# Optimization experiments

Hardware: AMD Instinct MI355X
Metric: run time of the kernel (lower is better)

Reference implementation:

```python
import jax, jax.numpy as jnp
import numpy as np

EPS = 1e-6
ALPHA = 0.1
BETA = 0.25


def setup_inputs() -> dict:
    key = jax.random.key(0)
    k1, k2, k3 = jax.random.split(key, 3)
    B, C, D = 4096, 256, 128
    x = jax.random.normal(k1, (B, D), dtype=jnp.float32)
    prev_q = jax.random.normal(k2, (B, D), dtype=jnp.float32)
    codes = jax.random.normal(k3, (1, C, D), dtype=jnp.float32)
    return {"x": x, "prev_q": prev_q, "codes": codes}


def compute_distance(x, codes):
    # x: (B, D); codes: (1, C, D) or (B, 1, D) -> (B, C) / (B, 1); metric='l2'
    return jnp.sum((x[:, None, :] - codes) ** 2, axis=-1)


def get_rotation_matrix(u, v, eps=EPS):
    # u: (B, D) normalized; v: (D,) normalized -> R: (B, D, D)
    B, D = u.shape
    uvT = u[:, :, None] * v[None, None, :]          # (B, D, D) = u v^T
    vuT = v[None, :, None] * u[:, None, :]          # (B, D, D) = v u^T
    A = uvT - vuT
    A2 = jnp.einsum('bik,bkj->bij', A, A)
    dot = jnp.einsum('bd,d->b', u, v)[:, None, None]
    I = jnp.eye(D, dtype=u.dtype)
    return I + A + A2 / (1.0 + dot + eps)


def reference(x, prev_q, codes):
    B, D = x.shape
    v = jnp.ones((D,), dtype=x.dtype) / jnp.sqrt(jnp.asarray(D, x.dtype))
    # F.normalize(prev_q, dim=-1, eps=1e-6)
    n = jnp.linalg.norm(prev_q, axis=-1, keepdims=True)
    u = prev_q / jnp.maximum(n, EPS)
    R = get_rotation_matrix(u, v)
    # x_canonical = R^T x
    x_canonical = jnp.einsum('bji,bj->bi', R, x)
    raw_distances = compute_distance(x_canonical, codes)        # (B, C)
    distances = raw_distances / D / ALPHA
    # eval path: argmin + gather
    indices = jnp.argmin(distances, axis=-1)                    # (B,)
    quantized_canonical = codes[0][indices]                     # (B, D)
    quantized = jnp.einsum('bij,bj->bi', R, quantized_canonical)
    loss_commit = compute_distance(x, jax.lax.stop_gradient(quantized)[:, None, :]).mean()
    loss_codebook = compute_distance(jax.lax.stop_gradient(x), quantized[:, None, :]).mean()
    loss = loss_commit + BETA * loss_codebook
    return quantized, indices, loss
```

## Files before the change

kernel.cpp:

```cpp
#include <hip/hip_runtime.h>

#define BD 4096
#define CD 256
#define DD 128
#define RB 16
#define TB 1024
#define SF 132

__global__ __launch_bounds__(TB) void rq_fused(
    const float* __restrict__ x,
    const float* __restrict__ pq,
    const float* __restrict__ codes,
    float* __restrict__ out)
{
    __shared__ float code_s[CD * SF];
    __shared__ float xc_s[RB * SF];
    __shared__ float row_c[RB], row_s[RB], row_invn[RB];
    __shared__ int   row_idx[RB];
    __shared__ float red_v[RB * 4];
    __shared__ int   red_i[RB * 4];
    __shared__ float loss_s[RB];

    const int tid  = threadIdx.x;
    const int wv   = tid >> 6;
    const int lane = tid & 63;
    const int row0 = blockIdx.x * RB;
    const float INV_SQRT_D = 0.088388347648318447f;

    {
        const float4* src = (const float4*)codes;
        #pragma unroll
        for (int k = 0; k < 8; k += 4) {
            const float4 t0 = src[(k + 0) * TB + tid];
            const float4 t1 = src[(k + 1) * TB + tid];
            const float4 t2 = src[(k + 2) * TB + tid];
            const float4 t3 = src[(k + 3) * TB + tid];
            int f;
            f = (k + 0) * TB + tid; *(float4*)(code_s + (f >> 5) * SF + (f & 31) * 4) = t0;
            f = (k + 1) * TB + tid; *(float4*)(code_s + (f >> 5) * SF + (f & 31) * 4) = t1;
            f = (k + 2) * TB + tid; *(float4*)(code_s + (f >> 5) * SF + (f & 31) * 4) = t2;
            f = (k + 3) * TB + tid; *(float4*)(code_s + (f >> 5) * SF + (f & 31) * 4) = t3;
        }
    }

    {
        const int r = wv;
        const size_t grow = (size_t)(row0 + r);
        const float2 xv = ((const float2*)(x  + grow * DD))[lane];
        const float2 pv = ((const float2*)(pq + grow * DD))[lane];
        float s0 = pv.x * pv.x + pv.y * pv.y;
        float s1 = pv.x + pv.y;
        float s2 = xv.x + xv.y;
        float s3 = pv.x * xv.x + pv.y * xv.y;
        #pragma unroll
        for (int m = 32; m > 0; m >>= 1) {
            s0 += __shfl_xor(s0, m);
            s1 += __shfl_xor(s1, m);
            s2 += __shfl_xor(s2, m);
            s3 += __shfl_xor(s3, m);
        }
        const float invn = 1.0f / fmaxf(sqrtf(s0), 1e-6f);
        const float b = s2 * INV_SQRT_D;
        const float a = s3 * invn;
        const float c = s1 * invn * INV_SQRT_D;
        const float s = 1.0f / (1.0f + c + 1e-6f);
        const float au = -b + s * (c * b - a);
        const float av =  a + s * (c * a - b);
        xc_s[r * SF + 2 * lane]     = xv.x + au * (pv.x * invn) + av * INV_SQRT_D;
        xc_s[r * SF + 2 * lane + 1] = xv.y + au * (pv.y * invn) + av * INV_SQRT_D;
        if (lane == 0) { row_c[r] = c; row_s[r] = s; row_invn[r] = invn; }
    }
    __syncthreads();

    const int rg = wv & 3;
    const int cq = wv >> 2;
    const int ci = cq * 64 + lane;
    const float* cp = code_s + ci * SF;
    const float* xb = xc_s + (rg * 4) * SF;
    float a0 = 0.f, a1 = 0.f, a2 = 0.f, a3 = 0.f;

    #pragma unroll 4
    for (int i = 0; i < 32; ++i) {
        const float4 q  = *(const float4*)(cp + i * 4);
        const float4 v0 = *(const float4*)(xb + 0 * SF + i * 4);
        const float4 v1 = *(const float4*)(xb + 1 * SF + i * 4);
        const float4 v2 = *(const float4*)(xb + 2 * SF + i * 4);
        const float4 v3 = *(const float4*)(xb + 3 * SF + i * 4);
        float dx;
        dx = v0.x - q.x; a0 = fmaf(dx, dx, a0);
        dx = v0.y - q.y; a0 = fmaf(dx, dx, a0);
        dx = v0.z - q.z; a0 = fmaf(dx, dx, a0);
        dx = v0.w - q.w; a0 = fmaf(dx, dx, a0);
        dx = v1.x - q.x; a1 = fmaf(dx, dx, a1);
        dx = v1.y - q.y; a1 = fmaf(dx, dx, a1);
        dx = v1.z - q.z; a1 = fmaf(dx, dx, a1);
        dx = v1.w - q.w; a1 = fmaf(dx, dx, a1);
        dx = v2.x - q.x; a2 = fmaf(dx, dx, a2);
        dx = v2.y - q.y; a2 = fmaf(dx, dx, a2);
        dx = v2.z - q.z; a2 = fmaf(dx, dx, a2);
        dx = v2.w - q.w; a2 = fmaf(dx, dx, a2);
        dx = v3.x - q.x; a3 = fmaf(dx, dx, a3);
        dx = v3.y - q.y; a3 = fmaf(dx, dx, a3);
        dx = v3.z - q.z; a3 = fmaf(dx, dx, a3);
        dx = v3.w - q.w; a3 = fmaf(dx, dx, a3);
    }

    float bv[4] = {a0, a1, a2, a3};
    int   bi[4] = {ci, ci, ci, ci};
    #pragma unroll
    for (int m = 1; m < 64; m <<= 1) {
        #pragma unroll
        for (int rr = 0; rr < 4; ++rr) {
            const float ov = __shfl_xor(bv[rr], m);
            const int   oi = __shfl_xor(bi[rr], m);
            if (ov < bv[rr] || (ov == bv[rr] && oi < bi[rr])) { bv[rr] = ov; bi[rr] = oi; }
        }
    }
    if (lane == 0) {
        #pragma unroll
        for (int rr = 0; rr < 4; ++rr) {
            red_v[(rg * 4 + rr) * 4 + cq] = bv[rr];
            red_i[(rg * 4 + rr) * 4 + cq] = bi[rr];
        }
    }
    __syncthreads();
    if (tid < RB) {
        float v0 = red_v[tid * 4]; int i0 = red_i[tid * 4];
        #pragma unroll
        for (int k = 1; k < 4; ++k) {
            const float ov = red_v[tid * 4 + k];
            const int   oi = red_i[tid * 4 + k];
            if (ov < v0 || (ov == v0 && oi < i0)) { v0 = ov; i0 = oi; }
        }
        row_idx[tid] = i0;
        out[(size_t)BD * DD + row0 + tid] = (float)i0;
    }
    __syncthreads();

    {
        const int r = wv;
        const int qi = row_idx[r];
        const float invn = row_invn[r];
        const float c = row_c[r];
        const float s = row_s[r];
        const size_t grow = (size_t)(row0 + r);
        const float2 q = ((const float2*)(code_s + qi * SF))[lane];
        const float2 p = ((const float2*)(pq + grow * DD))[lane];
        float pd = p.x * q.x + p.y * q.y;
        float ws = q.x + q.y;
        #pragma unroll
        for (int m = 32; m > 0; m >>= 1) {
            pd += __shfl_xor(pd, m);
            ws += __shfl_xor(ws, m);
        }
        const float pp = pd * invn;
        const float w  = ws * INV_SQRT_D;
        const float bu  =  w + s * (c * w - pp);
        const float bvv = -pp + s * (c * pp - w);
        float2 o;
        o.x = q.x + bu * (p.x * invn) + bvv * INV_SQRT_D;
        o.y = q.y + bu * (p.y * invn) + bvv * INV_SQRT_D;
        ((float2*)(out + grow * DD))[lane] = o;

        const float2 xv = ((const float2*)(x + grow * DD))[lane];
        float dx = xv.x - o.x;
        float ls = dx * dx;
        dx = xv.y - o.y;
        ls = fmaf(dx, dx, ls);
        #pragma unroll
        for (int m = 32; m > 0; m >>= 1) ls += __shfl_xor(ls, m);
        if (lane == 0) loss_s[r] = ls;
    }
    __syncthreads();
    if (tid == 0) {
        float tot = 0.f;
        #pragma unroll
        for (int r = 0; r < RB; ++r) tot += loss_s[r];
        atomicAdd(out + (size_t)BD * DD + BD, tot * (1.25f / (float)BD));
    }
}

extern "C" void kernel_launch(void* const* d_in, const int* in_sizes, int n_in,
                              void* d_out, int out_size, void* d_ws, size_t ws_size,
                              hipStream_t stream) {
    const float* xin   = (const float*)d_in[0];
    const float* prevq = (const float*)d_in[1];
    const float* codes = (const float*)d_in[2];
    float* out = (float*)d_out;
    hipMemsetAsync((void*)(out + (size_t)BD * DD + BD), 0, sizeof(float), stream);
    rq_fused<<<BD / RB, TB, 0, stream>>>(xin, prevq, codes, out);
}
```

Before: 77.47 us.

## Expand L2 distance algebraically using code norms and dot products with x and prev_q

Replaces the explicit canonical-vector distance with an expansion: ||c||^2 - 2 c·x - k1 c·p - k2 sum(c). The per-code norms and sums are precomputed in shared memory, and x and prev_q rows are read directly from global memory with wave-uniform addresses instead of from a shared xc buffer. This doubles the dot products per inner step and adds an extra sync and precompute pass. It also changes floating-point rounding, which could flip argmin decisions on near-ties.

```diff
diff --git a/kernel.cpp b/kernel.cpp
--- a/kernel.cpp
+++ b/kernel.cpp
@@ -14,8 +14,9 @@
     float* __restrict__ out)
 {
     __shared__ float code_s[CD * SF];
-    __shared__ float xc_s[RB * SF];
-    __shared__ float row_c[RB], row_s[RB], row_invn[RB];
+    __shared__ float cn2_s[CD];
+    __shared__ float csum_s[CD];
+    __shared__ float row_c[RB], row_s[RB], row_invn[RB], row_k1[RB], row_k2[RB];
     __shared__ int   row_idx[RB];
     __shared__ float red_v[RB * 4];
     __shared__ int   red_i[RB * 4];
@@ -66,47 +67,80 @@
         const float s = 1.0f / (1.0f + c + 1e-6f);
         const float au = -b + s * (c * b - a);
         const float av =  a + s * (c * a - b);
-        xc_s[r * SF + 2 * lane]     = xv.x + au * (pv.x * invn) + av * INV_SQRT_D;
-        xc_s[r * SF + 2 * lane + 1] = xv.y + au * (pv.y * invn) + av * INV_SQRT_D;
-        if (lane == 0) { row_c[r] = c; row_s[r] = s; row_invn[r] = invn; }
+        if (lane == 0) {
+            row_c[r] = c; row_s[r] = s; row_invn[r] = invn;
+            row_k1[r] = 2.0f * au * invn;
+            row_k2[r] = 2.0f * av * INV_SQRT_D;
+        }
+    }
+    __syncthreads();
+
+    if (tid < CD) {
+        const float* cp = code_s + tid * SF;
+        float n2 = 0.f, sm = 0.f;
+        #pragma unroll 8
+        for (int i = 0; i < 32; ++i) {
+            const float4 q = *(const float4*)(cp + i * 4);
+            n2 = fmaf(q.x, q.x, n2); n2 = fmaf(q.y, q.y, n2);
+            n2 = fmaf(q.z, q.z, n2); n2 = fmaf(q.w, q.w, n2);
+            sm += q.x + q.y + q.z + q.w;
+        }
+        cn2_s[tid] = n2; csum_s[tid] = sm;
     }
     __syncthreads();
 
     const int rg = wv & 3;
     const int cq = wv >> 2;
     const int ci = cq * 64 + lane;
+    const float cn2 = cn2_s[ci];
+    const float csm = csum_s[ci];
+    const int r0 = rg * 4;
+    const float k10 = row_k1[r0 + 0], k20 = row_k2[r0 + 0];
+    const float k11 = row_k1[r0 + 1], k21 = row_k2[r0 + 1];
+    const float k12 = row_k1[r0 + 2], k22 = row_k2[r0 + 2];
+    const float k13 = row_k1[r0 + 3], k23 = row_k2[r0 + 3];
+    const int grbase = __builtin_amdgcn_readfirstlane(row0 + r0);
+    const float* xb = x  + (size_t)grbase * DD;
+    const float* pb = pq + (size_t)grbase * DD;
     const float* cp = code_s + ci * SF;
-    const float* xb = xc_s + (rg * 4) * SF;
-    float a0 = 0.f, a1 = 0.f, a2 = 0.f, a3 = 0.f;
-
-    #pragma unroll 4
+    float ax0 = 0.f, ax1 = 0.f, ax2 = 0.f, ax3 = 0.f;
+    float ap0 = 0.f, ap1 = 0.f, ap2 = 0.f, ap3 = 0.f;
+
+    #pragma unroll 2
     for (int i = 0; i < 32; ++i) {
-        const float4 q  = *(const float4*)(cp + i * 4);
-        const float4 v0 = *(const float4*)(xb + 0 * SF + i * 4);
-        const float4 v1 = *(const float4*)(xb + 1 * SF + i * 4);
-        const float4 v2 = *(const float4*)(xb + 2 * SF + i * 4);
-        const float4 v3 = *(const float4*)(xb + 3 * SF + i * 4);
-        float dx;
-        dx = v0.x - q.x; a0 = fmaf(dx, dx, a0);
-        dx = v0.y - q.y; a0 = fmaf(dx, dx, a0);
-        dx = v0.z - q.z; a0 = fmaf(dx, dx, a0);
-        dx = v0.w - q.w; a0 = fmaf(dx, dx, a0);
-        dx = v1.x - q.x; a1 = fmaf(dx, dx, a1);
-        dx = v1.y - q.y; a1 = fmaf(dx, dx, a1);
-        dx = v1.z - q.z; a1 = fmaf(dx, dx, a1);
-        dx = v1.w - q.w; a1 = fmaf(dx, dx, a1);
-        dx = v2.x - q.x; a2 = fmaf(dx, dx, a2);
-        dx = v2.y - q.y; a2 = fmaf(dx, dx, a2);
-        dx = v2.z - q.z; a2 = fmaf(dx, dx, a2);
-        dx = v2.w - q.w; a2 = fmaf(dx, dx, a2);
-        dx = v3.x - q.x; a3 = fmaf(dx, dx, a3);
-        dx = v3.y - q.y; a3 = fmaf(dx, dx, a3);
-        dx = v3.z - q.z; a3 = fmaf(dx, dx, a3);
-        dx = v3.w - q.w; a3 = fmaf(dx, dx, a3);
-    }
-
-    float bv[4] = {a0, a1, a2, a3};
-    int   bi[4] = {ci, ci, ci, ci};
+        const float4 cv = *(const float4*)(cp + i * 4);
+        const float4 x0 = *(const float4*)(xb + 0 * DD + i * 4);
+        const float4 x1 = *(const float4*)(xb + 1 * DD + i * 4);
+        const float4 x2 = *(const float4*)(xb + 2 * DD + i * 4);
+        const float4 x3 = *(const float4*)(xb + 3 * DD + i * 4);
+        const float4 p0 = *(const float4*)(pb + 0 * DD + i * 4);
+        const float4 p1 = *(const float4*)(pb + 1 * DD + i * 4);
+        const float4 p2 = *(const float4*)(pb + 2 * DD + i * 4);
+        const float4 p3 = *(const float4*)(pb + 3 * DD + i * 4);
+        ax0 = fmaf(cv.x, x0.x, ax0); ax0 = fmaf(cv.y, x0.y, ax0);
+        ax0 = fmaf(cv.z, x0.z, ax0); ax0 = fmaf(cv.w, x0.w, ax0);
+        ap0 = fmaf(cv.x, p0.x, ap0); ap0 = fmaf(cv.y, p0.y, ap0);
+        ap0 = fmaf(cv.z, p0.z, ap0); ap0 = fmaf(cv.w, p0.w, ap0);
+        ax1 = fmaf(cv.x, x1.x, ax1); ax1 = fmaf(cv.y, x1.y, ax1);
+        ax1 = fmaf(cv.z, x1.z, ax1); ax1 = fmaf(cv.w, x1.w, ax1);
+        ap1 = fmaf(cv.x, p1.x, ap1); ap1 = fmaf(cv.y, p1.y, ap1);
+        ap1 = fmaf(cv.z, p1.z, ap1); ap1 = fmaf(cv.w, p1.w, ap1);
+        ax2 = fmaf(cv.x, x2.x, ax2); ax2 = fmaf(cv.y, x2.y, ax2);
+        ax2 = fmaf(cv.z, x2.z, ax2); ax2 = fmaf(cv.w, x2.w, ax2);
+        ap2 = fmaf(cv.x, p2.x, ap2); ap2 = fmaf(cv.y, p2.y, ap2);
+        ap2 = fmaf(cv.z, p2.z, ap2); ap2 = fmaf(cv.w, p2.w, ap2);
+        ax3 = fmaf(cv.x, x3.x, ax3); ax3 = fmaf(cv.y, x3.y, ax3);
+        ax3 = fmaf(cv.z, x3.z, ax3); ax3 = fmaf(cv.w, x3.w, ax3);
+        ap3 = fmaf(cv.x, p3.x, ap3); ap3 = fmaf(cv.y, p3.y, ap3);
+        ap3 = fmaf(cv.z, p3.z, ap3); ap3 = fmaf(cv.w, p3.w, ap3);
+    }
+
+    float bv[4]; int bi[4];
+    bv[0] = cn2 - 2.0f * ax0 - k10 * ap0 - k20 * csm;
+    bv[1] = cn2 - 2.0f * ax1 - k11 * ap1 - k21 * csm;
+    bv[2] = cn2 - 2.0f * ax2 - k12 * ap2 - k22 * csm;
+    bv[3] = cn2 - 2.0f * ax3 - k13 * ap3 - k23 * csm;
+    bi[0] = ci; bi[1] = ci; bi[2] = ci; bi[3] = ci;
     #pragma unroll
     for (int m = 1; m < 64; m <<= 1) {
         #pragma unroll
@@ -119,8 +153,8 @@
     if (lane == 0) {
         #pragma unroll
         for (int rr = 0; rr < 4; ++rr) {
-            red_v[(rg * 4 + rr) * 4 + cq] = bv[rr];
-            red_i[(rg * 4 + rr) * 4 + cq] = bi[rr];
+            red_v[(r0 + rr) * 4 + cq] = bv[rr];
+            red_i[(r0 + rr) * 4 + cq] = bi[rr];
         }
     }
     __syncthreads();
```

Result: slower. 81.04 us (+4.6%).

## Use dot-product expansion for L2 distances with split-K across wave halves

Applied to the files above, without the earlier changes.

Replaces the direct (x-c)^2 accumulation with ||c||^2 - 2·x·c, precomputing code norms in shared memory. Each wave now computes a 4-row × 2-code register tile over half of D, and the two halves are merged through shared memory that reuses the codebook buffer. Because that buffer is overwritten, the final gather reads the chosen code from global memory. This trades fewer subtracts and better register reuse for extra barriers, the partial-sum exchange and a small risk of argmin ties changing under the different rounding.

```diff
diff --git a/kernel.cpp b/kernel.cpp
--- a/kernel.cpp
+++ b/kernel.cpp
@@ -13,13 +13,25 @@
     const float* __restrict__ codes,
     float* __restrict__ out)
 {
-    __shared__ float code_s[CD * SF];
-    __shared__ float xc_s[RB * SF];
-    __shared__ float row_c[RB], row_s[RB], row_invn[RB];
-    __shared__ int   row_idx[RB];
-    __shared__ float red_v[RB * 4];
-    __shared__ int   red_i[RB * 4];
-    __shared__ float loss_s[RB];
+    __shared__ __align__(16) char pool[CD * SF * 4
+                                       + RB * DD * 4
+                                       + CD * 4
+                                       + RB * 4 * 4
+                                       + RB * 4
+                                       + RB * 2 * 8
+                                       + RB * 4];
+    float* code_s = (float*)pool;
+    float* mbuf   = (float*)pool;
+    float* xc_s   = (float*)(pool + CD * SF * 4);
+    float* cn2_s  = xc_s + RB * DD;
+    float* row_c  = cn2_s + CD;
+    float* row_s  = row_c + RB;
+    float* row_invn = row_s + RB;
+    float* row_pad  = row_invn + RB;  (void)row_pad;
+    int*   row_idx  = (int*)(row_invn + 2 * RB);
+    float* red_v    = (float*)(row_idx + RB);
+    int*   red_i    = (int*)(red_v + RB * 2);
+    float* loss_s   = (float*)(red_i + RB * 2);
 
     const int tid  = threadIdx.x;
     const int wv   = tid >> 6;
@@ -66,72 +78,114 @@
         const float s = 1.0f / (1.0f + c + 1e-6f);
         const float au = -b + s * (c * b - a);
         const float av =  a + s * (c * a - b);
-        xc_s[r * SF + 2 * lane]     = xv.x + au * (pv.x * invn) + av * INV_SQRT_D;
-        xc_s[r * SF + 2 * lane + 1] = xv.y + au * (pv.y * invn) + av * INV_SQRT_D;
+        float2 o;
+        o.x = xv.x + au * (pv.x * invn) + av * INV_SQRT_D;
+        o.y = xv.y + au * (pv.y * invn) + av * INV_SQRT_D;
+        ((float2*)(xc_s + r * DD))[lane] = o;
         if (lane == 0) { row_c[r] = c; row_s[r] = s; row_invn[r] = invn; }
     }
     __syncthreads();
 
-    const int rg = wv & 3;
-    const int cq = wv >> 2;
-    const int ci = cq * 64 + lane;
-    const float* cp = code_s + ci * SF;
-    const float* xb = xc_s + (rg * 4) * SF;
+    {
+        const int c = tid >> 2, q = tid & 3;
+        const float* cp = code_s + c * SF + q * 32;
+        float n2 = 0.f;
+        #pragma unroll
+        for (int i = 0; i < 8; ++i) {
+            const float4 v = *(const float4*)(cp + i * 4);
+            n2 = fmaf(v.x, v.x, n2); n2 = fmaf(v.y, v.y, n2);
+            n2 = fmaf(v.z, v.z, n2); n2 = fmaf(v.w, v.w, n2);
+        }
+        n2 += __shfl_xor(n2, 1);
+        n2 += __shfl_xor(n2, 2);
+        if (q == 0) cn2_s[c] = n2;
+    }
+    __syncthreads();
+
+    const int wgrp = wv & 7, half = wv >> 3;
+    const int rg = wgrp & 3, ch = wgrp >> 2;
+    const float* cb = code_s + (ch * 128 + lane) * SF + half * 64;
+    const float* xb = xc_s + (rg * 4) * DD + half * 64;
     float a0 = 0.f, a1 = 0.f, a2 = 0.f, a3 = 0.f;
+    float a4 = 0.f, a5 = 0.f, a6 = 0.f, a7 = 0.f;
 
     #pragma unroll 4
-    for (int i = 0; i < 32; ++i) {
-        const float4 q  = *(const float4*)(cp + i * 4);
-        const float4 v0 = *(const float4*)(xb + 0 * SF + i * 4);
-        const float4 v1 = *(const float4*)(xb + 1 * SF + i * 4);
-        const float4 v2 = *(const float4*)(xb + 2 * SF + i * 4);
-        const float4 v3 = *(const float4*)(xb + 3 * SF + i * 4);
-        float dx;
-        dx = v0.x - q.x; a0 = fmaf(dx, dx, a0);
-        dx = v0.y - q.y; a0 = fmaf(dx, dx, a0);
-        dx = v0.z - q.z; a0 = fmaf(dx, dx, a0);
-        dx = v0.w - q.w; a0 = fmaf(dx, dx, a0);
-        dx = v1.x - q.x; a1 = fmaf(dx, dx, a1);
-        dx = v1.y - q.y; a1 = fmaf(dx, dx, a1);
-        dx = v1.z - q.z; a1 = fmaf(dx, dx, a1);
-        dx = v1.w - q.w; a1 = fmaf(dx, dx, a1);
-        dx = v2.x - q.x; a2 = fmaf(dx, dx, a2);
-        dx = v2.y - q.y; a2 = fmaf(dx, dx, a2);
-        dx = v2.z - q.z; a2 = fmaf(dx, dx, a2);
-        dx = v2.w - q.w; a2 = fmaf(dx, dx, a2);
-        dx = v3.x - q.x; a3 = fmaf(dx, dx, a3);
-        dx = v3.y - q.y; a3 = fmaf(dx, dx, a3);
-        dx = v3.z - q.z; a3 = fmaf(dx, dx, a3);
-        dx = v3.w - q.w; a3 = fmaf(dx, dx, a3);
-    }
-
-    float bv[4] = {a0, a1, a2, a3};
-    int   bi[4] = {ci, ci, ci, ci};
-    #pragma unroll
-    for (int m = 1; m < 64; m <<= 1) {
-        #pragma unroll
-        for (int rr = 0; rr < 4; ++rr) {
-            const float ov = __shfl_xor(bv[rr], m);
-            const int   oi = __shfl_xor(bi[rr], m);
-            if (ov < bv[rr] || (ov == bv[rr] && oi < bi[rr])) { bv[rr] = ov; bi[rr] = oi; }
-        }
-    }
-    if (lane == 0) {
-        #pragma unroll
-        for (int rr = 0; rr < 4; ++rr) {
-            red_v[(rg * 4 + rr) * 4 + cq] = bv[rr];
-            red_i[(rg * 4 + rr) * 4 + cq] = bi[rr];
+    for (int i = 0; i < 16; ++i) {
+        const float4 c0 = *(const float4*)(cb + i * 4);
+        const float4 c1 = *(const float4*)(cb + 64 * SF + i * 4);
+        const float4 x0 = *(const float4*)(xb + 0 * DD + i * 4);
+        const float4 x1 = *(const float4*)(xb + 1 * DD + i * 4);
+        const float4 x2 = *(const float4*)(xb + 2 * DD + i * 4);
+        const float4 x3 = *(const float4*)(xb + 3 * DD + i * 4);
+        a0 = fmaf(c0.x, x0.x, a0); a0 = fmaf(c0.y, x0.y, a0);
+        a0 = fmaf(c0.z, x0.z, a0); a0 = fmaf(c0.w, x0.w, a0);
+        a1 = fmaf(c1.x, x0.x, a1); a1 = fmaf(c1.y, x0.y, a1);
+        a1 = fmaf(c1.z, x0.z, a1); a1 = fmaf(c1.w, x0.w, a1);
+        a2 = fmaf(c0.x, x1.x, a2); a2 = fmaf(c0.y, x1.y, a2);
+        a2 = fmaf(c0.z, x1.z, a2); a2 = fmaf(c0.w, x1.w, a2);
+        a3 = fmaf(c1.x, x1.x, a3); a3 = fmaf(c1.y, x1.y, a3);
+        a3 = fmaf(c1.z, x1.z, a3); a3 = fmaf(c1.w, x1.w, a3);
+        a4 = fmaf(c0.x, x2.x, a4); a4 = fmaf(c0.y, x2.y, a4);
+        a4 = fmaf(c0.z, x2.z, a4); a4 = fmaf(c0.w, x2.w, a4);
+        a5 = fmaf(c1.x, x2.x, a5); a5 = fmaf(c1.y, x2.y, a5);
+        a5 = fmaf(c1.z, x2.z, a5); a5 = fmaf(c1.w, x2.w, a5);
+        a6 = fmaf(c0.x, x3.x, a6); a6 = fmaf(c0.y, x3.y, a6);
+        a6 = fmaf(c0.z, x3.z, a6); a6 = fmaf(c0.w, x3.w, a6);
+        a7 = fmaf(c1.x, x3.x, a7); a7 = fmaf(c1.y, x3.y, a7);
+        a7 = fmaf(c1.z, x3.z, a7); a7 = fmaf(c1.w, x3.w, a7);
+    }
+
+    __syncthreads();
+    if (half == 1) {
+        float* mb = mbuf + ((size_t)wgrp * 64 + lane) * 8;
+        float4 v;
+        v.x = a0; v.y = a1; v.z = a2; v.w = a3; *(float4*)(mb)     = v;
+        v.x = a4; v.y = a5; v.z = a6; v.w = a7; *(float4*)(mb + 4) = v;
+    }
+    __syncthreads();
+    if (half == 0) {
+        const float* mb = mbuf + ((size_t)wgrp * 64 + lane) * 8;
+        const float4 m0 = *(const float4*)(mb);
+        const float4 m1 = *(const float4*)(mb + 4);
+        a0 += m0.x; a1 += m0.y; a2 += m0.z; a3 += m0.w;
+        a4 += m1.x; a5 += m1.y; a6 += m1.z; a7 += m1.w;
+        const int c0i = ch * 128 + lane;
+        const int c1i = c0i + 64;
+        const float cn20 = cn2_s[c0i];
+        const float cn21 = cn2_s[c1i];
+        float bv[4]; int bi[4];
+        {
+            const float s00 = fmaf(-2.f, a0, cn20), s01 = fmaf(-2.f, a1, cn21);
+            const float s10 = fmaf(-2.f, a2, cn20), s11 = fmaf(-2.f, a3, cn21);
+            const float s20 = fmaf(-2.f, a4, cn20), s21 = fmaf(-2.f, a5, cn21);
+            const float s30 = fmaf(-2.f, a6, cn20), s31 = fmaf(-2.f, a7, cn21);
+            if (s01 < s00) { bv[0] = s01; bi[0] = c1i; } else { bv[0] = s00; bi[0] = c0i; }
+            if (s11 < s10) { bv[1] = s11; bi[1] = c1i; } else { bv[1] = s10; bi[1] = c0i; }
+            if (s21 < s20) { bv[2] = s21; bi[2] = c1i; } else { bv[2] = s20; bi[2] = c0i; }
+            if (s31 < s30) { bv[3] = s31; bi[3] = c1i; } else { bv[3] = s30; bi[3] = c0i; }
+        }
+        #pragma unroll
+        for (int m = 1; m < 64; m <<= 1) {
+            #pragma unroll
+            for (int rr = 0; rr < 4; ++rr) {
+                const float ov = __shfl_xor(bv[rr], m);
+                const int   oi = __shfl_xor(bi[rr], m);
+                if (ov < bv[rr] || (ov == bv[rr] && oi < bi[rr])) { bv[rr] = ov; bi[rr] = oi; }
+            }
+        }
+        if (lane == 0) {
+            #pragma unroll
+            for (int rr = 0; rr < 4; ++rr) {
+                red_v[(rg * 4 + rr) * 2 + ch] = bv[rr];
+                red_i[(rg * 4 + rr) * 2 + ch] = bi[rr];
+            }
         }
     }
     __syncthreads();
     if (tid < RB) {
-        float v0 = red_v[tid * 4]; int i0 = red_i[tid * 4];
-        #pragma unroll
-        for (int k = 1; k < 4; ++k) {
-            const float ov = red_v[tid * 4 + k];
-            const int   oi = red_i[tid * 4 + k];
-            if (ov < v0 || (ov == v0 && oi < i0)) { v0 = ov; i0 = oi; }
-        }
+        float v0 = red_v[tid * 2]; int i0 = red_i[tid * 2];
+        const float v1 = red_v[tid * 2 + 1]; const int i1 = red_i[tid * 2 + 1];
+        if (v1 < v0 || (v1 == v0 && i1 < i0)) { v0 = v1; i0 = i1; }
         row_idx[tid] = i0;
         out[(size_t)BD * DD + row0 + tid] = (float)i0;
     }
@@ -144,7 +198,7 @@
         const float c = row_c[r];
         const float s = row_s[r];
         const size_t grow = (size_t)(row0 + r);
-        const float2 q = ((const float2*)(code_s + qi * SF))[lane];
+        const float2 q = ((const float2*)(codes + (size_t)qi * DD))[lane];
         const float2 p = ((const float2*)(pq + grow * DD))[lane];
         float pd = p.x * q.x + p.y * q.y;
         float ws = q.x + q.y;
```

Result: faster. 74.45 us (-3.9%).

## Register-tile distance as dot products with split-K across waves and shared-memory merge

Applied to the files above, without the earlier changes.

The distance loop becomes a 4x4 register tile of row-by-code dot products plus code norms, computed as ||c||^2 - 2 x·c. The D dimension is split across four wave groups, and partial sums are merged through shared memory that reuses the codebook buffer. Only one wave group then runs the argmin, which removes the separate cross-wave reduction stage. Because the codebook buffer is overwritten, the final gather now reads the chosen code from global memory. In exchange there is an extra synchronization and merge pass, and the dot-product form can change argmin tie-breaking in floating point.

```diff
diff --git a/kernel.cpp b/kernel.cpp
--- a/kernel.cpp
+++ b/kernel.cpp
@@ -13,13 +13,19 @@
     const float* __restrict__ codes,
     float* __restrict__ out)
 {
-    __shared__ float code_s[CD * SF];
-    __shared__ float xc_s[RB * SF];
-    __shared__ float row_c[RB], row_s[RB], row_invn[RB];
-    __shared__ int   row_idx[RB];
-    __shared__ float red_v[RB * 4];
-    __shared__ int   red_i[RB * 4];
-    __shared__ float loss_s[RB];
+    __shared__ __align__(16) char pool[CD * SF * 4
+                                       + RB * DD * 4
+                                       + RB * 3 * 4
+                                       + RB * 4
+                                       + RB * 4];
+    float* code_s   = (float*)pool;
+    float* mbuf     = (float*)pool;
+    float* xc_s     = (float*)(pool + CD * SF * 4);
+    float* row_c    = xc_s + RB * DD;
+    float* row_s    = row_c + RB;
+    float* row_invn = row_s + RB;
+    int*   row_idx  = (int*)(row_invn + RB);
+    float* loss_s   = (float*)(row_idx + RB);
 
     const int tid  = threadIdx.x;
     const int wv   = tid >> 6;
@@ -66,74 +72,146 @@
         const float s = 1.0f / (1.0f + c + 1e-6f);
         const float au = -b + s * (c * b - a);
         const float av =  a + s * (c * a - b);
-        xc_s[r * SF + 2 * lane]     = xv.x + au * (pv.x * invn) + av * INV_SQRT_D;
-        xc_s[r * SF + 2 * lane + 1] = xv.y + au * (pv.y * invn) + av * INV_SQRT_D;
+        float2 o;
+        o.x = xv.x + au * (pv.x * invn) + av * INV_SQRT_D;
+        o.y = xv.y + au * (pv.y * invn) + av * INV_SQRT_D;
+        ((float2*)(xc_s + r * DD))[lane] = o;
         if (lane == 0) { row_c[r] = c; row_s[r] = s; row_invn[r] = invn; }
     }
     __syncthreads();
 
     const int rg = wv & 3;
-    const int cq = wv >> 2;
-    const int ci = cq * 64 + lane;
-    const float* cp = code_s + ci * SF;
-    const float* xb = xc_s + (rg * 4) * SF;
-    float a0 = 0.f, a1 = 0.f, a2 = 0.f, a3 = 0.f;
-
-    #pragma unroll 4
-    for (int i = 0; i < 32; ++i) {
-        const float4 q  = *(const float4*)(cp + i * 4);
-        const float4 v0 = *(const float4*)(xb + 0 * SF + i * 4);
-        const float4 v1 = *(const float4*)(xb + 1 * SF + i * 4);
-        const float4 v2 = *(const float4*)(xb + 2 * SF + i * 4);
-        const float4 v3 = *(const float4*)(xb + 3 * SF + i * 4);
-        float dx;
-        dx = v0.x - q.x; a0 = fmaf(dx, dx, a0);
-        dx = v0.y - q.y; a0 = fmaf(dx, dx, a0);
-        dx = v0.z - q.z; a0 = fmaf(dx, dx, a0);
-        dx = v0.w - q.w; a0 = fmaf(dx, dx, a0);
-        dx = v1.x - q.x; a1 = fmaf(dx, dx, a1);
-        dx = v1.y - q.y; a1 = fmaf(dx, dx, a1);
-        dx = v1.z - q.z; a1 = fmaf(dx, dx, a1);
-        dx = v1.w - q.w; a1 = fmaf(dx, dx, a1);
-        dx = v2.x - q.x; a2 = fmaf(dx, dx, a2);
-        dx = v2.y - q.y; a2 = fmaf(dx, dx, a2);
-        dx = v2.z - q.z; a2 = fmaf(dx, dx, a2);
-        dx = v2.w - q.w; a2 = fmaf(dx, dx, a2);
-        dx = v3.x - q.x; a3 = fmaf(dx, dx, a3);
-        dx = v3.y - q.y; a3 = fmaf(dx, dx, a3);
-        dx = v3.z - q.z; a3 = fmaf(dx, dx, a3);
-        dx = v3.w - q.w; a3 = fmaf(dx, dx, a3);
-    }
-
-    float bv[4] = {a0, a1, a2, a3};
-    int   bi[4] = {ci, ci, ci, ci};
-    #pragma unroll
-    for (int m = 1; m < 64; m <<= 1) {
-        #pragma unroll
-        for (int rr = 0; rr < 4; ++rr) {
-            const float ov = __shfl_xor(bv[rr], m);
-            const int   oi = __shfl_xor(bi[rr], m);
-            if (ov < bv[rr] || (ov == bv[rr] && oi < bi[rr])) { bv[rr] = ov; bi[rr] = oi; }
-        }
-    }
-    if (lane == 0) {
-        #pragma unroll
-        for (int rr = 0; rr < 4; ++rr) {
-            red_v[(rg * 4 + rr) * 4 + cq] = bv[rr];
-            red_i[(rg * 4 + rr) * 4 + cq] = bi[rr];
-        }
-    }
-    __syncthreads();
-    if (tid < RB) {
-        float v0 = red_v[tid * 4]; int i0 = red_i[tid * 4];
-        #pragma unroll
-        for (int k = 1; k < 4; ++k) {
-            const float ov = red_v[tid * 4 + k];
-            const int   oi = red_i[tid * 4 + k];
-            if (ov < v0 || (ov == v0 && oi < i0)) { v0 = ov; i0 = oi; }
-        }
-        row_idx[tid] = i0;
-        out[(size_t)BD * DD + row0 + tid] = (float)i0;
+    const int q  = wv >> 2;
+    const float* cb = code_s + lane * SF + q * 32;
+    const float* xb = xc_s + (rg * 4) * DD + q * 32;
+    float d00 = 0.f, d01 = 0.f, d02 = 0.f, d03 = 0.f;
+    float d10 = 0.f, d11 = 0.f, d12 = 0.f, d13 = 0.f;
+    float d20 = 0.f, d21 = 0.f, d22 = 0.f, d23 = 0.f;
+    float d30 = 0.f, d31 = 0.f, d32 = 0.f, d33 = 0.f;
+    float n20 = 0.f, n21 = 0.f, n22 = 0.f, n23 = 0.f;
+
+    #pragma unroll 2
+    for (int i = 0; i < 8; ++i) {
+        const float4 c0 = *(const float4*)(cb + 0 * 64 * SF + i * 4);
+        const float4 c1 = *(const float4*)(cb + 1 * 64 * SF + i * 4);
+        const float4 c2 = *(const float4*)(cb + 2 * 64 * SF + i * 4);
+        const float4 c3 = *(const float4*)(cb + 3 * 64 * SF + i * 4);
+        const float4 x0 = *(const float4*)(xb + 0 * DD + i * 4);
+        const float4 x1 = *(const float4*)(xb + 1 * DD + i * 4);
+        const float4 x2 = *(const float4*)(xb + 2 * DD + i * 4);
+        const float4 x3 = *(const float4*)(xb + 3 * DD + i * 4);
+        n20 = fmaf(c0.x, c0.x, n20); n20 = fmaf(c0.y, c0.y, n20);
+        n20 = fmaf(c0.z, c0.z, n20); n20 = fmaf(c0.w, c0.w, n20);
+        n21 = fmaf(c1.x, c1.x, n21); n21 = fmaf(c1.y, c1.y, n21);
+        n21 = fmaf(c1.z, c1.z, n21); n21 = fmaf(c1.w, c1.w, n21);
+        n22 = fmaf(c2.x, c2.x, n22); n22 = fmaf(c2.y, c2.y, n22);
+        n22 = fmaf(c2.z, c2.z, n22); n22 = fmaf(c2.w, c2.w, n22);
+        n23 = fmaf(c3.x, c3.x, n23); n23 = fmaf(c3.y, c3.y, n23);
+        n23 = fmaf(c3.z, c3.z, n23); n23 = fmaf(c3.w, c3.w, n23);
+        d00 = fmaf(c0.x, x0.x, d00); d00 = fmaf(c0.y, x0.y, d00);
+        d00 = fmaf(c0.z, x0.z, d00); d00 = fmaf(c0.w, x0.w, d00);
+        d01 = fmaf(c1.x, x0.x, d01); d01 = fmaf(c1.y, x0.y, d01);
+        d01 = fmaf(c1.z, x0.z, d01); d01 = fmaf(c1.w, x0.w, d01);
+        d02 = fmaf(c2.x, x0.x, d02); d02 = fmaf(c2.y, x0.y, d02);
+        d02 = fmaf(c2.z, x0.z, d02); d02 = fmaf(c2.w, x0.w, d02);
+        d03 = fmaf(c3.x, x0.x, d03); d03 = fmaf(c3.y, x0.y, d03);
+        d03 = fmaf(c3.z, x0.z, d03); d03 = fmaf(c3.w, x0.w, d03);
+        d10 = fmaf(c0.x, x1.x, d10); d10 = fmaf(c0.y, x1.y, d10);
+        d10 = fmaf(c0.z, x1.z, d10); d10 = fmaf(c0.w, x1.w, d10);
+        d11 = fmaf(c1.x, x1.x, d11); d11 = fmaf(c1.y, x1.y, d11);
+        d11 = fmaf(c1.z, x1.z, d11); d11 = fmaf(c1.w, x1.w, d11);
+        d12 = fmaf(c2.x, x1.x, d12); d12 = fmaf(c2.y, x1.y, d12);
+        d12 = fmaf(c2.z, x1.z, d12); d12 = fmaf(c2.w, x1.w, d12);
+        d13 = fmaf(c3.x, x1.x, d13); d13 = fmaf(c3.y, x1.y, d13);
+        d13 = fmaf(c3.z, x1.z, d13); d13 = fmaf(c3.w, x1.w, d13);
+        d20 = fmaf(c0.x, x2.x, d20); d20 = fmaf(c0.y, x2.y, d20);
+        d20 = fmaf(c0.z, x2.z, d20); d20 = fmaf(c0.w, x2.w, d20);
+        d21 = fmaf(c1.x, x2.x, d21); d21 = fmaf(c1.y, x2.y, d21);
+        d21 = fmaf(c1.z, x2.z, d21); d21 = fmaf(c1.w, x2.w, d21);
+        d22 = fmaf(c2.x, x2.x, d22); d22 = fmaf(c2.y, x2.y, d22);
+        d22 = fmaf(c2.z, x2.z, d22); d22 = fmaf(c2.w, x2.w, d22);
+        d23 = fmaf(c3.x, x2.x, d23); d23 = fmaf(c3.y, x2.y, d23);
+        d23 = fmaf(c3.z, x2.z, d23); d23 = fmaf(c3.w, x2.w, d23);
+        d30 = fmaf(c0.x, x3.x, d30); d30 = fmaf(c0.y, x3.y, d30);
+        d30 = fmaf(c0.z, x3.z, d30); d30 = fmaf(c0.w, x3.w, d30);
+        d31 = fmaf(c1.x, x3.x, d31); d31 = fmaf(c1.y, x3.y, d31);
+        d31 = fmaf(c1.z, x3.z, d31); d31 = fmaf(c1.w, x3.w, d31);
+        d32 = fmaf(c2.x, x3.x, d32); d32 = fmaf(c2.y, x3.y, d32);
+        d32 = fmaf(c2.z, x3.z, d32); d32 = fmaf(c2.w, x3.w, d32);
+        d33 = fmaf(c3.x, x3.x, d33); d33 = fmaf(c3.y, x3.y, d33);
+        d33 = fmaf(c3.z, x3.z, d33); d33 = fmaf(c3.w, x3.w, d33);
+    }
+
+    __syncthreads();
+    if (q != 0) {
+        float* mb = mbuf + (size_t)(((q - 1) * 4 + rg) * 64 + lane) * 20;
+        float4 v;
+        v.x = d00; v.y = d01; v.z = d02; v.w = d03; *(float4*)(mb)      = v;
+        v.x = d10; v.y = d11; v.z = d12; v.w = d13; *(float4*)(mb + 4)  = v;
+        v.x = d20; v.y = d21; v.z = d22; v.w = d23; *(float4*)(mb + 8)  = v;
+        v.x = d30; v.y = d31; v.z = d32; v.w = d33; *(float4*)(mb + 12) = v;
+        v.x = n20; v.y = n21; v.z = n22; v.w = n23; *(float4*)(mb + 16) = v;
+    }
+    __syncthreads();
+    if (q == 0) {
+        #pragma unroll
+        for (int p = 0; p < 3; ++p) {
+            const float* mb = mbuf + (size_t)((p * 4 + rg) * 64 + lane) * 20;
+            const float4 m0 = *(const float4*)(mb);
+            const float4 m1 = *(const float4*)(mb + 4);
+            const float4 m2 = *(const float4*)(mb + 8);
+            const float4 m3 = *(const float4*)(mb + 12);
+            const float4 m4 = *(const float4*)(mb + 16);
+            d00 += m0.x; d01 += m0.y; d02 += m0.z; d03 += m0.w;
+            d10 += m1.x; d11 += m1.y; d12 += m1.z; d13 += m1.w;
+            d20 += m2.x; d21 += m2.y; d22 += m2.z; d23 += m2.w;
+            d30 += m3.x; d31 += m3.y; d32 += m3.z; d33 += m3.w;
+            n20 += m4.x; n21 += m4.y; n22 += m4.z; n23 += m4.w;
+        }
+        float bv[4]; int bi[4];
+        {
+            float s0, s1, s2, s3;
+            s0 = fmaf(-2.f, d00, n20); s1 = fmaf(-2.f, d01, n21);
+            s2 = fmaf(-2.f, d02, n22); s3 = fmaf(-2.f, d03, n23);
+            bv[0] = s0; bi[0] = lane;
+            if (s1 < bv[0]) { bv[0] = s1; bi[0] = lane + 64; }
+            if (s2 < bv[0]) { bv[0] = s2; bi[0] = lane + 128; }
+            if (s3 < bv[0]) { bv[0] = s3; bi[0] = lane + 192; }
+            s0 = fmaf(-2.f, d10, n20); s1 = fmaf(-2.f, d11, n21);
+            s2 = fmaf(-2.f, d12, n22); s3 = fmaf(-2.f, d13, n23);
+            bv[1] = s0; bi[1] = lane;
+            if (s1 < bv[1]) { bv[1] = s1; bi[1] = lane + 64; }
+            if (s2 < bv[1]) { bv[1] = s2; bi[1] = lane + 128; }
+            if (s3 < bv[1]) { bv[1] = s3; bi[1] = lane + 192; }
+            s0 = fmaf(-2.f, d20, n20); s1 = fmaf(-2.f, d21, n21);
+            s2 = fmaf(-2.f, d22, n22); s3 = fmaf(-2.f, d23, n23);
+            bv[2] = s0; bi[2] = lane;
+            if (s1 < bv[2]) { bv[2] = s1; bi[2] = lane + 64; }
+            if (s2 < bv[2]) { bv[2] = s2; bi[2] = lane + 128; }
+            if (s3 < bv[2]) { bv[2] = s3; bi[2] = lane + 192; }
+            s0 = fmaf(-2.f, d30, n20); s1 = fmaf(-2.f, d31, n21);
+            s2 = fmaf(-2.f, d32, n22); s3 = fmaf(-2.f, d33, n23);
+            bv[3] = s0; bi[3] = lane;
+            if (s1 < bv[3]) { bv[3] = s1; bi[3] = lane + 64; }
+            if (s2 < bv[3]) { bv[3] = s2; bi[3] = lane + 128; }
+            if (s3 < bv[3]) { bv[3] = s3; bi[3] = lane + 192; }
+        }
+        #pragma unroll
+        for (int m = 1; m < 64; m <<= 1) {
+            #pragma unroll
+            for (int rr = 0; rr < 4; ++rr) {
+                const float ov = __shfl_xor(bv[rr], m);
+                const int   oi = __shfl_xor(bi[rr], m);
+                if (ov < bv[rr] || (ov == bv[rr] && oi < bi[rr])) { bv[rr] = ov; bi[rr] = oi; }
+            }
+        }
+        if (lane == 0) {
+            #pragma unroll
+            for (int rr = 0; rr < 4; ++rr) {
+                row_idx[rg * 4 + rr] = bi[rr];
+                out[(size_t)BD * DD + row0 + rg * 4 + rr] = (float)bi[rr];
+            }
+        }
     }
     __syncthreads();
 
@@ -144,10 +222,10 @@
         const float c = row_c[r];
         const float s = row_s[r];
         const size_t grow = (size_t)(row0 + r);
-        const float2 q = ((const float2*)(code_s + qi * SF))[lane];
-        const float2 p = ((const float2*)(pq + grow * DD))[lane];
-        float pd = p.x * q.x + p.y * q.y;
-        float ws = q.x + q.y;
+        const float2 qv = ((const float2*)(codes + (size_t)qi * DD))[lane];
+        const float2 p  = ((const float2*)(pq + grow * DD))[lane];
+        float pd = p.x * qv.x + p.y * qv.y;
+        float ws = qv.x + qv.y;
         #pragma unroll
         for (int m = 32; m > 0; m >>= 1) {
             pd += __shfl_xor(pd, m);
@@ -158,8 +236,8 @@
         const float bu  =  w + s * (c * w - pp);
         const float bvv = -pp + s * (c * pp - w);
         float2 o;
-        o.x = q.x + bu * (p.x * invn) + bvv * INV_SQRT_D;
-        o.y = q.y + bu * (p.y * invn) + bvv * INV_SQRT_D;
+        o.x = qv.x + bu * (p.x * invn) + bvv * INV_SQRT_D;
+        o.y = qv.y + bu * (p.y * invn) + bvv * INV_SQRT_D;
         ((float2*)(out + grow * DD))[lane] = o;
 
         const float2 xv = ((const float2*)(x + grow * DD))[lane];
```

Result: no change. 78.27 us (+1.0%).
